# Optimization experiments

Hardware: AMD Instinct MI355X
Metric: run time of the kernel (lower is better)

## Reference

```python
import jax, jax.numpy as jnp
import numpy as np

B, D, E, H = 2048, 1024, 16, 4096
NUM_ACTIVE = 2
LN_EPS = 1e-5
NORM_EPS = 1e-12


def setup_inputs() -> dict:
    key = jax.random.key(0)
    ks = jax.random.split(key, 4)
    s1 = 1.0 / np.sqrt(D)
    s2 = 1.0 / np.sqrt(H)
    return {
        "input": jax.random.normal(ks[0], (B, D), jnp.float32),
        "ln_gamma": jnp.ones((D,), jnp.float32),
        "ln_beta": jnp.zeros((D,), jnp.float32),
        "expert_keys": jax.random.normal(ks[1], (D, E), jnp.float32),
        "W1": jax.random.normal(ks[2], (E, D, H), jnp.float32) * s1,
        "b1": jnp.zeros((E, H), jnp.float32),
        "W2": jax.random.normal(ks[3], (E, H, D), jnp.float32) * s2,
        "b2": jnp.zeros((E, D), jnp.float32),
    }


def reference(input, ln_gamma, ln_beta, expert_keys, W1, b1, W2, b2):
    # Gating: LayerNorm(input) @ normalize(expert_keys, dim=-1)
    mu = jnp.mean(input, axis=-1, keepdims=True)
    var = jnp.mean((input - mu) ** 2, axis=-1, keepdims=True)
    xn = (input - mu) / jnp.sqrt(var + LN_EPS) * ln_gamma + ln_beta
    # F.normalize(expert_keys, dim=-1): each row (per feature) normalized over experts
    keys = expert_keys / jnp.clip(
        jnp.linalg.norm(expert_keys, axis=-1, keepdims=True), NORM_EPS)
    logits = xn @ keys  # [B, E]
    # Top-k routing (argsort descending, take first num_active)
    top_vals, top_ids = jax.lax.top_k(logits, NUM_ACTIVE)  # [B, k]
    gates_k = jax.nn.softmax(top_vals, axis=-1)            # softmax over chosen logits
    gates = jnp.zeros_like(logits).at[
        jnp.arange(logits.shape[0])[:, None], top_ids].set(gates_k)  # [B, E]
    # Experts applied to RAW input (not the normalized gating input), dense-all-experts
    h = jax.nn.relu(jnp.einsum('bd,edh->beh', input, W1) + b1)   # [B, E, H]
    eo = jnp.einsum('beh,ehd->bed', h, W2) + b2                  # [B, E, D]
    # Weighted combine: only top-k experts have nonzero gates
    out = jnp.einsum('bed,be->bd', eo, gates)                    # [B, D]
    return out
```

## Files before the change

### kernel.cpp

```cpp
#include <hip/hip_runtime.h>
#include <hip/hip_bf16.h>
#include <cstdint>
#include <cstddef>

#define D_ 1024
#define H_ 4096
#define E_ 16
#define B_ 2048

constexpr int CAP = 384;

typedef __attribute__((ext_vector_type(4))) float f32x4;
typedef __attribute__((ext_vector_type(8))) short bf16x8;

__device__ __forceinline__ unsigned pack2(float a, float b) {
  __hip_bfloat162 h = __float22bfloat162_rn(make_float2(a, b));
  union { __hip_bfloat162 h2; unsigned u; } cv; cv.h2 = h;
  return cv.u;
}
__device__ __forceinline__ float bflo(unsigned u) { return __uint_as_float(u << 16); }
__device__ __forceinline__ float bfhi(unsigned u) { return __uint_as_float(u & 0xffff0000u); }

#define GLL16(g, l)                                                         \
  __builtin_amdgcn_global_load_lds(                                         \
      (const __attribute__((address_space(1))) void*)(g),                   \
      (__attribute__((address_space(3))) void*)(l), 16, 0, 0)

#define WAITV(n) asm volatile("s_waitcnt vmcnt(" #n ")" ::: "memory")
#define WAITL()  asm volatile("s_waitcnt lgkmcnt(0)" ::: "memory")
#define BAR() __builtin_amdgcn_s_barrier()

__global__ void moe_zero(int* __restrict__ cnt) {
  if (threadIdx.x < E_) cnt[threadIdx.x] = 0;
}

__global__ __launch_bounds__(256) void moe_gating3(
    const float* __restrict__ x, const float* __restrict__ gamma,
    const float* __restrict__ beta, const float* __restrict__ keys,
    int* __restrict__ cnt, int4* __restrict__ rmi, float2* __restrict__ rmg,
    unsigned short* __restrict__ xg)
{
  const int b = blockIdx.x, t = threadIdx.x;
  const int w = t >> 6;
  const float4 xv = ((const float4*)(x + (size_t)b * D_))[t];
  float s  = xv.x + xv.y + xv.z + xv.w;
  float sq = xv.x*xv.x + xv.y*xv.y + xv.z*xv.z + xv.w*xv.w;
#pragma unroll
  for (int off = 32; off >= 1; off >>= 1) {
    s  += __shfl_down(s, off);
    sq += __shfl_down(sq, off);
  }
  __shared__ float ssum[4], ssq[4], sstat[2];
  if ((t & 63) == 0) { ssum[w] = s; ssq[w] = sq; }
  __syncthreads();
  if (t == 0) {
    float S = ssum[0] + ssum[1] + ssum[2] + ssum[3];
    float Q = ssq[0] + ssq[1] + ssq[2] + ssq[3];
    float mu  = S * (1.0f / D_);
    float var = Q * (1.0f / D_) - mu * mu;
    sstat[0] = mu; sstat[1] = rsqrtf(var + 1e-5f);
  }
  __syncthreads();
  const float mu = sstat[0], rstd = sstat[1];
  const float4 gv = ((const float4*)gamma)[t];
  const float4 bv = ((const float4*)beta)[t];
  float xn[4] = {(xv.x-mu)*rstd*gv.x+bv.x, (xv.y-mu)*rstd*gv.y+bv.y,
                 (xv.z-mu)*rstd*gv.z+bv.z, (xv.w-mu)*rstd*gv.w+bv.w};
  float acc[E_];
#pragma unroll
  for (int e2 = 0; e2 < E_; ++e2) acc[e2] = 0.f;
#pragma unroll
  for (int j = 0; j < 4; ++j) {
    const int d = 4*t + j;
    const float* kr = keys + (size_t)d * E_;
    float kv[E_];
#pragma unroll
    for (int e2 = 0; e2 < E_; ++e2) kv[e2] = kr[e2];
    float nq = 0.f;
#pragma unroll
    for (int e2 = 0; e2 < E_; ++e2) nq += kv[e2] * kv[e2];
    const float sc = xn[j] / fmaxf(sqrtf(nq), 1e-12f);
#pragma unroll
    for (int e2 = 0; e2 < E_; ++e2) acc[e2] += sc * kv[e2];
  }
#pragma unroll
  for (int off = 1; off < 64; off <<= 1) {
#pragma unroll
    for (int e2 = 0; e2 < E_; ++e2) acc[e2] += __shfl_xor(acc[e2], off);
  }
  __shared__ float wred[4][E_];
  if ((t & 63) == 0) {
#pragma unroll
    for (int e2 = 0; e2 < E_; ++e2) wred[w][e2] = acc[e2];
  }
  __syncthreads();
  __shared__ int sE[2], sP[2];
  if (t == 0) {
    float lg[E_];
#pragma unroll
    for (int e2 = 0; e2 < E_; ++e2)
      lg[e2] = wred[0][e2] + wred[1][e2] + wred[2][e2] + wred[3][e2];
    float v0 = -1e30f; int e0 = 0;
    for (int e2 = 0; e2 < E_; ++e2) { if (lg[e2] > v0) { v0 = lg[e2]; e0 = e2; } }
    float v1 = -1e30f; int e1 = 0;
    for (int e2 = 0; e2 < E_; ++e2) { if (e2 == e0) continue; if (lg[e2] > v1) { v1 = lg[e2]; e1 = e2; } }
    const float g0 = 1.f / (1.f + __expf(v1 - v0));
    const float g1 = 1.f - g0;
    int p0 = atomicAdd(cnt + e0, 1); if (p0 >= CAP) p0 = CAP - 1;
    int p1 = atomicAdd(cnt + e1, 1); if (p1 >= CAP) p1 = CAP - 1;
    rmi[b] = make_int4(e0, p0, e1, p1);
    rmg[b] = make_float2(g0, g1);
    sE[0] = e0; sP[0] = p0;
    sE[1] = e1; sP[1] = p1;
  }
  __syncthreads();
  const uint2 pk = make_uint2(pack2(xv.x, xv.y), pack2(xv.z, xv.w));
#pragma unroll
  for (int i = 0; i < 2; ++i)
    ((uint2*)(xg + ((size_t)sE[i] * CAP + sP[i]) * D_))[t] = pk;
}

template<int KROW, int KLEN, int NTILE, int WN, int SPLITK, bool RELU>
__global__ void __launch_bounds__(256, 3)
moe_gemm(const unsigned short* __restrict__ Asrc, const float* __restrict__ W,
         const float* __restrict__ bias, const int* __restrict__ cnt,
         unsigned short* __restrict__ d0, unsigned short* __restrict__ d1,
         unsigned short* __restrict__ d2, unsigned short* __restrict__ d3)
{
  constexpr int NPHASE = KLEN / 32;
  constexpr int NT = WN / NTILE;
  constexpr int MT = 2;
  constexpr int CF = NTILE / 64;

  const int bx = blockIdx.x;
  const int xcd = bx & 7;
  int slot = bx >> 3;
  const int mt = slot % MT; slot /= MT;
  const int nt = slot % NT; slot /= NT;
  const int eh = slot & 1;
  const int part = slot >> 1;
  const int e  = (xcd << 1) | eh;
  const int nb = nt * NTILE;
  const int koff = part * KLEN;
  unsigned short* dst = (part == 0) ? d0 : (part == 1) ? d1 : (part == 2) ? d2 : d3;

  int cntE = cnt[e]; if (cntE > CAP) cntE = CAP;
  if (mt * 192 >= cntE) return;

  const int t = threadIdx.x, w = t >> 6, lane = t & 63;
  const int l15 = lane & 15, l4 = lane >> 4;

  __shared__ __align__(16) unsigned short As[2][192 * 32];
  __shared__ __align__(16) unsigned short Bs[2][NTILE * 40];

  asm volatile("s_waitcnt vmcnt(0) lgkmcnt(0)" ::: "memory");

  const unsigned short* Ae = Asrc + (size_t)e * CAP * KROW + (size_t)mt * 192 * KROW + koff;
  const float* We = W + (size_t)e * KROW * WN + (size_t)koff * WN + nb;

  const unsigned short *srcA0, *srcA1, *srcA2;
  {
    const int c0 = t,        r0 = c0 >> 2;
    const int c1 = t + 256,  r1 = c1 >> 2;
    const int c2 = t + 512,  r2 = c2 >> 2;
    srcA0 = Ae + (size_t)r0 * KROW + ((c0 & 3) ^ ((r0 >> 1) & 3)) * 8;
    srcA1 = Ae + (size_t)r1 * KROW + ((c1 & 3) ^ ((r1 >> 1) & 3)) * 8;
    srcA2 = Ae + (size_t)r2 * KROW + ((c2 & 3) ^ ((r2 >> 1) & 3)) * 8;
  }
  const float* srcB = We + (size_t)(w * 8) * WN + lane;
  int bofs[CF];
#pragma unroll
  for (int h = 0; h < CF; ++h) {
    const int n = h * 64 + lane;
    bofs[h] = (80 * n + 16 * w) ^ (((n >> 3) & 3) << 4);
  }

  float R0[CF][8], R1[CF][8];

#define ISSUE(p, Rv, BUF) do {                                              \
    const float* bp_ = srcB + (size_t)(p) * 32 * WN;                        \
    _Pragma("unroll")                                                       \
    for (int h = 0; h < CF; ++h)                                            \
      _Pragma("unroll")                                                     \
      for (int j = 0; j < 8; ++j)                                           \
        Rv[h][j] = bp_[(size_t)j * WN + h * 64];                            \
    const int ko_ = (p) * 32;                                               \
    GLL16(srcA0 + ko_, &As[BUF][(0 * 256 + w * 64) * 8]);                   \
    GLL16(srcA1 + ko_, &As[BUF][(1 * 256 + w * 64) * 8]);                   \
    GLL16(srcA2 + ko_, &As[BUF][(2 * 256 + w * 64) * 8]);                   \
  } while (0)

#define WAIT_OLD() do {                                                     \
    if constexpr (CF == 2) { WAITV(19); } else { WAITV(11); }               \
  } while (0)

#define WRITE(Rv, BUF) do {                                                 \
    _Pragma("unroll")                                                       \
    for (int h = 0; h < CF; ++h) {                                          \
      uint4 q_;                                                             \
      q_.x = pack2(Rv[h][0], Rv[h][1]);                                     \
      q_.y = pack2(Rv[h][2], Rv[h][3]);                                     \
      q_.z = pack2(Rv[h][4], Rv[h][5]);                                     \
      q_.w = pack2(Rv[h][6], Rv[h][7]);                                     \
      *(uint4*)((char*)&Bs[BUF][0] + bofs[h]) = q_;                         \
    }                                                                       \
  } while (0)

  f32x4 acc[12][CF];
#pragma unroll
  for (int rf = 0; rf < 12; ++rf)
#pragma unroll
    for (int cf = 0; cf < CF; ++cf) acc[rf][cf] = f32x4{0,0,0,0};

  const int swA = (l15 >> 1) & 3;
  const int mrow0 = mt * 192;

#define COMP(BUF) do {                                                      \
    bf16x8 BB[CF];                                                          \
    _Pragma("unroll")                                                       \
    for (int cf = 0; cf < CF; ++cf) {                                       \
      const int n_ = w * (16 * CF) + cf * 16 + l15;                         \
      BB[cf] = *(const bf16x8*)((const char*)&Bs[BUF][0]                    \
               + ((80 * n_ + 16 * l4) ^ (((n_ >> 3) & 3) << 4)));           \
    }                                                                       \
    __builtin_amdgcn_s_setprio(1);                                          \
    _Pragma("unroll")                                                       \
    for (int rf = 0; rf < 12; ++rf) {                                       \
      if (mrow0 + rf * 16 < cntE) {                                         \
        const bf16x8 a = *(const bf16x8*)&As[BUF][((rf * 16 + l15) * 4 + (l4 ^ swA)) * 8]; \
        _Pragma("unroll")                                                   \
        for (int cf = 0; cf < CF; ++cf)                                     \
          acc[rf][cf] = __builtin_amdgcn_mfma_f32_16x16x32_bf16(a, BB[cf], acc[rf][cf], 0,0,0); \
      }                                                                     \
    }                                                                       \
    __builtin_amdgcn_s_setprio(0);                                          \
  } while (0)

  ISSUE(0, R0, 0);
#pragma unroll 1
  for (int p = 0; p < NPHASE; p += 2) {
    ISSUE(p + 1, R1, 1);
    WAIT_OLD();
    WRITE(R0, 0); WAITL(); BAR();
    COMP(0); BAR();
    if (p + 2 < NPHASE) { ISSUE(p + 2, R0, 0); WAIT_OLD(); }
    else { WAITV(0); }
    WRITE(R1, 1); WAITL(); BAR();
    COMP(1); BAR();
  }
#undef ISSUE
#undef WAIT_OLD
#undef WRITE
#undef COMP

  unsigned short* dbase = dst + (size_t)e * CAP * WN + nb + w * (16 * CF);
#pragma unroll
  for (int rf = 0; rf < 12; ++rf) {
    if (mrow0 + rf * 16 >= cntE && rf > 0) continue;
#pragma unroll
    for (int cf = 0; cf < CF; ++cf) {
      float bv = 0.f;
      if constexpr (RELU) bv = bias[e * WN + nb + w * (16 * CF) + cf * 16 + l15];
#pragma unroll
      for (int r = 0; r < 4; ++r) {
        const int row = mrow0 + rf * 16 + l4 * 4 + r;
        float v = acc[rf][cf][r];
        if constexpr (RELU) v = fmaxf(v + bv, 0.f);
        const unsigned u01 = pack2(v, __shfl_xor(v, 1));
        const float uo = __shfl_xor(__uint_as_float(u01), 2);
        if ((l15 & 3) == 0)
          *(uint2*)(dbase + (size_t)row * WN + cf * 16 + l15) =
              make_uint2(u01, __float_as_uint(uo));
      }
    }
  }
}

__global__ __launch_bounds__(256) void moe_comb(
    const unsigned short* __restrict__ p0, const unsigned short* __restrict__ p1,
    const unsigned short* __restrict__ p2, const unsigned short* __restrict__ p3,
    const float* __restrict__ b2, const int4* __restrict__ rmi,
    const float2* __restrict__ rmg, float* __restrict__ out)
{
  const int b = blockIdx.x, t = threadIdx.x;
  const int4 m = rmi[b];
  const float2 g = rmg[b];
  const int c = t * 4;
  const size_t offA = ((size_t)m.x * CAP + m.y) * D_ + c;
  const size_t offB = ((size_t)m.z * CAP + m.w) * D_ + c;
  float a0, a1, a2, a3, c0, c1, c2, c3;
  {
    const uint2 ua = *(const uint2*)(p0 + offA);
    const uint2 ub = *(const uint2*)(p0 + offB);
    a0 = bflo(ua.x); a1 = bfhi(ua.x); a2 = bflo(ua.y); a3 = bfhi(ua.y);
    c0 = bflo(ub.x); c1 = bfhi(ub.x); c2 = bflo(ub.y); c3 = bfhi(ub.y);
  }
  const unsigned short* parts[3] = { p1, p2, p3 };
#pragma unroll
  for (int i = 0; i < 3; ++i) {
    if (parts[i] != nullptr) {
      const uint2 ua = *(const uint2*)(parts[i] + offA);
      const uint2 ub = *(const uint2*)(parts[i] + offB);
      a0 += bflo(ua.x); a1 += bfhi(ua.x); a2 += bflo(ua.y); a3 += bfhi(ua.y);
      c0 += bflo(ub.x); c1 += bfhi(ub.x); c2 += bflo(ub.y); c3 += bfhi(ub.y);
    }
  }
  const float4 b2a = *(const float4*)(b2 + (size_t)m.x * D_ + c);
  const float4 b2b = *(const float4*)(b2 + (size_t)m.z * D_ + c);
  float4 o;
  o.x = g.x * (a0 + b2a.x) + g.y * (c0 + b2b.x);
  o.y = g.x * (a1 + b2a.y) + g.y * (c1 + b2b.y);
  o.z = g.x * (a2 + b2a.z) + g.y * (c2 + b2b.z);
  o.w = g.x * (a3 + b2a.w) + g.y * (c3 + b2b.w);
  *(float4*)(out + (size_t)b * D_ + c) = o;
}

extern "C" void kernel_launch(void* const* d_in, const int* in_sizes, int n_in,
                              void* d_out, int out_size, void* d_ws, size_t ws_size,
                              hipStream_t stream) {
  const float* x     = (const float*)d_in[0];
  const float* gamma = (const float*)d_in[1];
  const float* beta  = (const float*)d_in[2];
  const float* keys  = (const float*)d_in[3];
  const float* W1    = (const float*)d_in[4];
  const float* b1    = (const float*)d_in[5];
  const float* W2    = (const float*)d_in[6];
  const float* b2    = (const float*)d_in[7];
  float* out = (float*)d_out;

  char* ws = (char*)d_ws;
  const size_t OFF_RMI = 256;
  const size_t OFF_RMG = OFF_RMI + (size_t)B_ * 16;
  const size_t OFF_XG  = OFF_RMG + (size_t)B_ * 8;
  const size_t EO_SZ   = (size_t)E_ * CAP * D_ * 2;
  const size_t OFF_HW  = OFF_XG + EO_SZ;
  const size_t HW_SZ   = (size_t)E_ * CAP * H_ * 2;
  const size_t OFF_EO1 = OFF_HW + HW_SZ;
  const size_t NEED2   = OFF_EO1 + EO_SZ;
  const size_t NEED4   = OFF_EO1 + 3 * EO_SZ;

  int*    cnt = (int*)ws;
  int4*   rmi = (int4*)(ws + OFF_RMI);
  float2* rmg = (float2*)(ws + OFF_RMG);
  unsigned short* xg  = (unsigned short*)(ws + OFF_XG);
  unsigned short* eo0 = xg;
  unsigned short* hws = (unsigned short*)(ws + OFF_HW);

  moe_zero<<<1, 64, 0, stream>>>(cnt);
  moe_gating3<<<B_, 256, 0, stream>>>(x, gamma, beta, keys, cnt, rmi, rmg, xg);

  moe_gemm<D_, D_, 128, H_, 1, true><<<1024, 256, 0, stream>>>(
      xg, W1, b1, cnt, hws, nullptr, nullptr, nullptr);

  if (ws_size >= NEED4) {
    unsigned short* eo1 = (unsigned short*)(ws + OFF_EO1);
    unsigned short* eo2 = (unsigned short*)(ws + OFF_EO1 + EO_SZ);
    unsigned short* eo3 = (unsigned short*)(ws + OFF_EO1 + 2 * EO_SZ);
    moe_gemm<H_, H_ / 4, 128, D_, 4, false><<<1024, 256, 0, stream>>>(
        hws, W2, nullptr, cnt, eo0, eo1, eo2, eo3);
    moe_comb<<<B_, 256, 0, stream>>>(eo0, eo1, eo2, eo3, b2, rmi, rmg, out);
  } else if (ws_size >= NEED2) {
    unsigned short* eo1 = (unsigned short*)(ws + OFF_EO1);
    moe_gemm<H_, H_ / 2, 64, D_, 2, false><<<1024, 256, 0, stream>>>(
        hws, W2, nullptr, cnt, eo0, eo1, nullptr, nullptr);
    moe_comb<<<B_, 256, 0, stream>>>(eo0, eo1, nullptr, nullptr, b2, rmi, rmg, out);
  } else {
    moe_gemm<H_, H_, 64, D_, 1, false><<<512, 256, 0, stream>>>(
        hws, W2, nullptr, cnt, eo0, nullptr, nullptr, nullptr);
    moe_comb<<<B_, 256, 0, stream>>>(eo0, nullptr, nullptr, nullptr, b2, rmi, rmg, out);
  }
}
```

Before: 313.1 us.

## Stream fp32 weights directly to LDS and shrink GEMM N-tile to 64

Measured after the change: 333.5 us. +6.5%, slower.

```diff
diff --git a/kernel.cpp b/kernel.cpp
--- a/kernel.cpp
+++ b/kernel.cpp
@@ -27,7 +27,6 @@
       (__attribute__((address_space(3))) void*)(l), 16, 0, 0)
 
 #define WAITV(n) asm volatile("s_waitcnt vmcnt(" #n ")" ::: "memory")
-#define WAITL()  asm volatile("s_waitcnt lgkmcnt(0)" ::: "memory")
 #define BAR() __builtin_amdgcn_s_barrier()
 
 __global__ void moe_zero(int* __restrict__ cnt) {
@@ -120,27 +119,26 @@
     ((uint2*)(xg + ((size_t)sE[i] * CAP + sP[i]) * D_))[t] = pk;
 }
 
-template<int KROW, int KLEN, int NTILE, int WN, int SPLITK, bool RELU>
-__global__ void __launch_bounds__(256, 3)
+template<int KROW, int KLEN, int WN, int SPLITK, bool RELU>
+__global__ void __launch_bounds__(256, 4)
 moe_gemm(const unsigned short* __restrict__ Asrc, const float* __restrict__ W,
          const float* __restrict__ bias, const int* __restrict__ cnt,
          unsigned short* __restrict__ d0, unsigned short* __restrict__ d1,
          unsigned short* __restrict__ d2, unsigned short* __restrict__ d3)
 {
   constexpr int NPHASE = KLEN / 32;
-  constexpr int NT = WN / NTILE;
+  constexpr int NT = WN / 64;
   constexpr int MT = 2;
-  constexpr int CF = NTILE / 64;
 
   const int bx = blockIdx.x;
   const int xcd = bx & 7;
   int slot = bx >> 3;
   const int mt = slot % MT; slot /= MT;
   const int nt = slot % NT; slot /= NT;
-  const int eh = slot & 1;
-  const int part = slot >> 1;
+  const int eh = slot & 1;  slot >>= 1;
+  const int part = slot;
   const int e  = (xcd << 1) | eh;
-  const int nb = nt * NTILE;
+  const int nb = nt * 64;
   const int koff = part * KLEN;
   unsigned short* dst = (part == 0) ? d0 : (part == 1) ? d1 : (part == 2) ? d2 : d3;
 
@@ -151,7 +149,7 @@
   const int l15 = lane & 15, l4 = lane >> 4;
 
   __shared__ __align__(16) unsigned short As[2][192 * 32];
-  __shared__ __align__(16) unsigned short Bs[2][NTILE * 40];
+  __shared__ __align__(16) float Bs[2][2048];
 
   asm volatile("s_waitcnt vmcnt(0) lgkmcnt(0)" ::: "memory");
 
@@ -167,111 +165,81 @@
     srcA1 = Ae + (size_t)r1 * KROW + ((c1 & 3) ^ ((r1 >> 1) & 3)) * 8;
     srcA2 = Ae + (size_t)r2 * KROW + ((c2 & 3) ^ ((r2 >> 1) & 3)) * 8;
   }
-  const float* srcB = We + (size_t)(w * 8) * WN + lane;
-  int bofs[CF];
-#pragma unroll
-  for (int h = 0; h < CF; ++h) {
-    const int n = h * 64 + lane;
-    bofs[h] = (80 * n + 16 * w) ^ (((n >> 3) & 3) << 4);
-  }
-
-  float R0[CF][8], R1[CF][8];
-
-#define ISSUE(p, Rv, BUF) do {                                              \
-    const float* bp_ = srcB + (size_t)(p) * 32 * WN;                        \
-    _Pragma("unroll")                                                       \
-    for (int h = 0; h < CF; ++h)                                            \
-      _Pragma("unroll")                                                     \
-      for (int j = 0; j < 8; ++j)                                           \
-        Rv[h][j] = bp_[(size_t)j * WN + h * 64];                            \
+  const float *srcB0, *srcB1;
+  {
+    const int kr0 = w * 8 + (lane >> 4);
+    const int c4  = (lane & 15) ^ (w << 2);
+    srcB0 = We + (size_t)kr0 * WN + c4 * 4;
+    srcB1 = srcB0 + (size_t)4 * WN;
+  }
+
+#define ISSUE(p, BUF) do {                                                  \
     const int ko_ = (p) * 32;                                               \
     GLL16(srcA0 + ko_, &As[BUF][(0 * 256 + w * 64) * 8]);                   \
     GLL16(srcA1 + ko_, &As[BUF][(1 * 256 + w * 64) * 8]);                   \
     GLL16(srcA2 + ko_, &As[BUF][(2 * 256 + w * 64) * 8]);                   \
+    GLL16(srcB0 + (size_t)ko_ * WN, &Bs[BUF][w * 512]);                     \
+    GLL16(srcB1 + (size_t)ko_ * WN, &Bs[BUF][w * 512 + 256]);               \
   } while (0)
 
-#define WAIT_OLD() do {                                                     \
-    if constexpr (CF == 2) { WAITV(19); } else { WAITV(11); }               \
-  } while (0)
-
-#define WRITE(Rv, BUF) do {                                                 \
-    _Pragma("unroll")                                                       \
-    for (int h = 0; h < CF; ++h) {                                          \
-      uint4 q_;                                                             \
-      q_.x = pack2(Rv[h][0], Rv[h][1]);                                     \
-      q_.y = pack2(Rv[h][2], Rv[h][3]);                                     \
-      q_.z = pack2(Rv[h][4], Rv[h][5]);                                     \
-      q_.w = pack2(Rv[h][6], Rv[h][7]);                                     \
-      *(uint4*)((char*)&Bs[BUF][0] + bofs[h]) = q_;                         \
-    }                                                                       \
-  } while (0)
-
-  f32x4 acc[12][CF];
-#pragma unroll
-  for (int rf = 0; rf < 12; ++rf)
-#pragma unroll
-    for (int cf = 0; cf < CF; ++cf) acc[rf][cf] = f32x4{0,0,0,0};
+  f32x4 acc[12];
+#pragma unroll
+  for (int rf = 0; rf < 12; ++rf) acc[rf] = f32x4{0,0,0,0};
 
   const int swA = (l15 >> 1) & 3;
   const int mrow0 = mt * 192;
+  const int ncol = w * 16 + l15;
+  const int bslot = (ncol >> 2) ^ (l4 << 2);
+  const int bbase = bslot * 4 + (ncol & 3);
 
 #define COMP(BUF) do {                                                      \
-    bf16x8 BB[CF];                                                          \
+    float bfv[8];                                                           \
     _Pragma("unroll")                                                       \
-    for (int cf = 0; cf < CF; ++cf) {                                       \
-      const int n_ = w * (16 * CF) + cf * 16 + l15;                         \
-      BB[cf] = *(const bf16x8*)((const char*)&Bs[BUF][0]                    \
-               + ((80 * n_ + 16 * l4) ^ (((n_ >> 3) & 3) << 4)));           \
-    }                                                                       \
+    for (int j2 = 0; j2 < 8; ++j2)                                          \
+      bfv[j2] = Bs[BUF][(l4 * 8 + j2) * 64 + bbase];                        \
+    union { unsigned u[4]; bf16x8 v; } BB;                                  \
+    _Pragma("unroll")                                                       \
+    for (int i2 = 0; i2 < 4; ++i2)                                          \
+      BB.u[i2] = pack2(bfv[2*i2], bfv[2*i2+1]);                             \
     __builtin_amdgcn_s_setprio(1);                                          \
     _Pragma("unroll")                                                       \
     for (int rf = 0; rf < 12; ++rf) {                                       \
       if (mrow0 + rf * 16 < cntE) {                                         \
         const bf16x8 a = *(const bf16x8*)&As[BUF][((rf * 16 + l15) * 4 + (l4 ^ swA)) * 8]; \
-        _Pragma("unroll")                                                   \
-        for (int cf = 0; cf < CF; ++cf)                                     \
-          acc[rf][cf] = __builtin_amdgcn_mfma_f32_16x16x32_bf16(a, BB[cf], acc[rf][cf], 0,0,0); \
+        acc[rf] = __builtin_amdgcn_mfma_f32_16x16x32_bf16(a, BB.v, acc[rf], 0,0,0); \
       }                                                                     \
     }                                                                       \
     __builtin_amdgcn_s_setprio(0);                                          \
   } while (0)
 
-  ISSUE(0, R0, 0);
+  ISSUE(0, 0);
 #pragma unroll 1
   for (int p = 0; p < NPHASE; p += 2) {
-    ISSUE(p + 1, R1, 1);
-    WAIT_OLD();
-    WRITE(R0, 0); WAITL(); BAR();
-    COMP(0); BAR();
-    if (p + 2 < NPHASE) { ISSUE(p + 2, R0, 0); WAIT_OLD(); }
+    ISSUE(p + 1, 1);
+    WAITV(5);
+    BAR(); COMP(0); BAR();
+    if (p + 2 < NPHASE) { ISSUE(p + 2, 0); WAITV(5); }
     else { WAITV(0); }
-    WRITE(R1, 1); WAITL(); BAR();
-    COMP(1); BAR();
+    BAR(); COMP(1); BAR();
   }
 #undef ISSUE
-#undef WAIT_OLD
-#undef WRITE
 #undef COMP
 
-  unsigned short* dbase = dst + (size_t)e * CAP * WN + nb + w * (16 * CF);
+  unsigned short* dbase = dst + (size_t)e * CAP * WN + nb + w * 16;
+  float bv = 0.f;
+  if constexpr (RELU) bv = bias[e * WN + nb + w * 16 + l15];
 #pragma unroll
   for (int rf = 0; rf < 12; ++rf) {
     if (mrow0 + rf * 16 >= cntE && rf > 0) continue;
 #pragma unroll
-    for (int cf = 0; cf < CF; ++cf) {
-      float bv = 0.f;
-      if constexpr (RELU) bv = bias[e * WN + nb + w * (16 * CF) + cf * 16 + l15];
-#pragma unroll
-      for (int r = 0; r < 4; ++r) {
-        const int row = mrow0 + rf * 16 + l4 * 4 + r;
-        float v = acc[rf][cf][r];
-        if constexpr (RELU) v = fmaxf(v + bv, 0.f);
-        const unsigned u01 = pack2(v, __shfl_xor(v, 1));
-        const float uo = __shfl_xor(__uint_as_float(u01), 2);
-        if ((l15 & 3) == 0)
-          *(uint2*)(dbase + (size_t)row * WN + cf * 16 + l15) =
-              make_uint2(u01, __float_as_uint(uo));
-      }
+    for (int r = 0; r < 4; ++r) {
+      const int row = mrow0 + rf * 16 + l4 * 4 + r;
+      float v = acc[rf][r];
+      if constexpr (RELU) v = fmaxf(v + bv, 0.f);
+      const unsigned u01 = pack2(v, __shfl_xor(v, 1));
+      const float uo = __shfl_xor(__uint_as_float(u01), 2);
+      if ((l15 & 3) == 0)
+        *(uint2*)(dbase + (size_t)row * WN + l15) = make_uint2(u01, __float_as_uint(uo));
     }
   }
 }
@@ -349,23 +317,23 @@
   moe_zero<<<1, 64, 0, stream>>>(cnt);
   moe_gating3<<<B_, 256, 0, stream>>>(x, gamma, beta, keys, cnt, rmi, rmg, xg);
 
-  moe_gemm<D_, D_, 128, H_, 1, true><<<1024, 256, 0, stream>>>(
+  moe_gemm<D_, D_, H_, 1, true><<<2048, 256, 0, stream>>>(
       xg, W1, b1, cnt, hws, nullptr, nullptr, nullptr);
 
   if (ws_size >= NEED4) {
     unsigned short* eo1 = (unsigned short*)(ws + OFF_EO1);
     unsigned short* eo2 = (unsigned short*)(ws + OFF_EO1 + EO_SZ);
     unsigned short* eo3 = (unsigned short*)(ws + OFF_EO1 + 2 * EO_SZ);
-    moe_gemm<H_, H_ / 4, 128, D_, 4, false><<<1024, 256, 0, stream>>>(
+    moe_gemm<H_, H_ / 4, D_, 4, false><<<2048, 256, 0, stream>>>(
         hws, W2, nullptr, cnt, eo0, eo1, eo2, eo3);
     moe_comb<<<B_, 256, 0, stream>>>(eo0, eo1, eo2, eo3, b2, rmi, rmg, out);
   } else if (ws_size >= NEED2) {
     unsigned short* eo1 = (unsigned short*)(ws + OFF_EO1);
-    moe_gemm<H_, H_ / 2, 64, D_, 2, false><<<1024, 256, 0, stream>>>(
+    moe_gemm<H_, H_ / 2, D_, 2, false><<<1024, 256, 0, stream>>>(
         hws, W2, nullptr, cnt, eo0, eo1, nullptr, nullptr);
     moe_comb<<<B_, 256, 0, stream>>>(eo0, eo1, nullptr, nullptr, b2, rmi, rmg, out);
   } else {
-    moe_gemm<H_, H_, 64, D_, 1, false><<<512, 256, 0, stream>>>(
+    moe_gemm<H_, H_, D_, 1, false><<<512, 256, 0, stream>>>(
         hws, W2, nullptr, cnt, eo0, nullptr, nullptr, nullptr);
     moe_comb<<<B_, 256, 0, stream>>>(eo0, nullptr, nullptr, nullptr, b2, rmi, rmg, out);
   }
```
